# Optimization experiments

Measured on AMD Instinct MI355X. Metric: run time of the kernel, lower is better.

Reference implementation:

```python
import jax, jax.numpy as jnp
import numpy as np

NUM_HEADS = 16


def setup_inputs() -> dict:
    key = jax.random.key(0)
    ks = jax.random.split(key, 5)
    B, N, C = 4, 2048, 1024
    x = jax.random.normal(ks[0], (B, N, C), dtype=jnp.float32)
    mask = jax.random.randint(ks[1], (B, N), 0, 2, dtype=jnp.int32)
    W_qkv = jax.random.normal(ks[2], (C, 3 * C), dtype=jnp.float32) * (C ** -0.5)
    W_proj = jax.random.normal(ks[3], (C, C), dtype=jnp.float32) * (C ** -0.5)
    b_proj = jnp.zeros((C,), dtype=jnp.float32)
    return {"x": x, "mask": mask, "W_qkv": W_qkv, "W_proj": W_proj, "b_proj": b_proj}


def reference(x, mask, W_qkv, W_proj, b_proj):
    B, N, C = x.shape
    H = NUM_HEADS
    hd = C // H
    scale = hd ** -0.5
    # qkv projection -> [3, B, H, N, hd]
    qkv = (x @ W_qkv).reshape(B, N, 3, H, hd).transpose(2, 0, 3, 1, 4)
    q, k, v = qkv[0], qkv[1], qkv[2]
    attn = jnp.einsum('bhqd,bhkd->bhqk', q, k) * scale  # [B,H,N,N]
    add_mask = (mask[:, None, None, :] != 1).astype(jnp.float32) * -10000.0
    attn = jax.nn.softmax(attn + add_mask, axis=-1)
    out = jnp.einsum('bhqk,bhkd->bhqd', attn, v)  # [B,H,N,hd]
    out = out.transpose(0, 2, 1, 3).reshape(B, N, C)
    return out @ W_proj + b_proj
```

## Files before the change

### kernel.cpp

```cpp
#include <hip/hip_runtime.h>

typedef unsigned short u16;
typedef unsigned int u32;
typedef unsigned long long u64;
typedef __attribute__((ext_vector_type(8))) short short8;
typedef __attribute__((ext_vector_type(4))) float f32x4;

#define QSCALE 0.18033688f

__device__ __forceinline__ u16 f2bf(float f) {
  u32 u = __builtin_bit_cast(u32, f);
  u += 0x7fffu + ((u >> 16) & 1u);
  return (u16)(u >> 16);
}

__device__ __forceinline__ float fexp2(float x) {
#if __has_builtin(__builtin_amdgcn_exp2f)
  return __builtin_amdgcn_exp2f(x);
#else
  return exp2f(x);
#endif
}

__device__ __forceinline__ void glds16(u16* lds, const u16* g) {
  __builtin_amdgcn_global_load_lds(
      (const __attribute__((address_space(1))) u32*)g,
      (__attribute__((address_space(3))) u32*)lds, 16, 0, 0);
}

#define MFMA(a, b, c) __builtin_amdgcn_mfma_f32_16x16x32_bf16((a), (b), (c), 0, 0, 0)


__global__ __launch_bounds__(256) void prep(const float* __restrict__ x,
                                            const int* __restrict__ mask,
                                            const float* __restrict__ Wqkv,
                                            const float* __restrict__ Wproj,
                                            u16* __restrict__ xb,
                                            u16* __restrict__ wqkvt,
                                            u16* __restrict__ wprojt,
                                            int* __restrict__ s2t,
                                            int* __restrict__ nkbuf) {
  __shared__ float tile[64][65];
  __shared__ int wtot[4];
  __shared__ int wbase[5];
  const int bid = blockIdx.x, t = threadIdx.x;

  if (bid < 8192) {
    int i = bid * 256 + t;
    float4 v = ((const float4*)x)[i];
    union { u16 s[4]; u64 ll; } u;
    u.s[0] = f2bf(v.x); u.s[1] = f2bf(v.y); u.s[2] = f2bf(v.z); u.s[3] = f2bf(v.w);
    ((u64*)xb)[i] = u.ll;
    return;
  }
  if (bid < 9216) {
    const float* Wm; u16* Wt; int Cc, bj, bi;
    if (bid < 8960) { int tt = bid - 8192; Wm = Wqkv;  Wt = wqkvt;  Cc = 3072; bj = tt % 48; bi = tt / 48; }
    else            { int tt = bid - 8960; Wm = Wproj; Wt = wprojt; Cc = 1024; bj = tt & 15; bi = tt >> 4; }
    const int r = t >> 4, c4 = (t & 15) << 2;
    for (int rr = r; rr < 64; rr += 16) {
      float4 v = *(const float4*)&Wm[(size_t)(bi * 64 + rr) * Cc + bj * 64 + c4];
      tile[rr][c4] = v.x; tile[rr][c4 + 1] = v.y; tile[rr][c4 + 2] = v.z; tile[rr][c4 + 3] = v.w;
    }
    __syncthreads();
    for (int rr = r; rr < 64; rr += 16) {
      union { u16 s[4]; u64 ll; } u;
      u.s[0] = f2bf(tile[c4][rr]);
      u.s[1] = f2bf(tile[c4 + 1][rr]);
      u.s[2] = f2bf(tile[c4 + 2][rr]);
      u.s[3] = f2bf(tile[c4 + 3][rr]);
      *(u64*)&Wt[(size_t)(bj * 64 + rr) * 1024 + bi * 64 + c4] = u.ll;
    }
    return;
  }
  const int b = bid - 9216;
  const int lane = t & 63, w = t >> 6;
  int m8[8], c = 0;
  #pragma unroll
  for (int j = 0; j < 8; j++) {
    m8[j] = (mask[b * 2048 + t * 8 + j] == 1);
    c += m8[j];
  }
  int incl = c;
  #pragma unroll
  for (int off = 1; off < 64; off <<= 1) {
    int v = __shfl_up(incl, off);
    if (lane >= off) incl += v;
  }
  if (lane == 63) wtot[w] = incl;
  __syncthreads();
  if (t == 0) {
    int s = 0;
    for (int i = 0; i < 4; i++) { wbase[i] = s; s += wtot[i]; }
    wbase[4] = s;
  }
  __syncthreads();
  const int nk = wbase[4];
  int urun = wbase[w] + incl - c;
  #pragma unroll
  for (int j = 0; j < 8; j++) {
    int tok = t * 8 + j;
    int slot = m8[j] ? urun : nk + (tok - urun);
    s2t[b * 2048 + slot] = b * 2048 + tok;
    urun += m8[j];
  }
  if (t == 0) nkbuf[b] = nk;
}

__global__ __launch_bounds__(256, 4) void gemm_fused(const u16* __restrict__ xb,
                                                     const u16* __restrict__ wqkvt,
                                                     const int* __restrict__ s2t,
                                                     const int* __restrict__ nkbuf,
                                                     u16* __restrict__ qbuf,
                                                     u16* __restrict__ kc,
                                                     u16* __restrict__ vtc) {
  __shared__ u16 Asm[128 * 64];
  __shared__ u16 Bsm[128 * 64];
  const int bid = blockIdx.x;
  const int role = bid >> 9;
  const int sub = bid & 511;
  const int tid = threadIdx.x, lane = tid & 63, w = tid >> 6;
  const int quad = lane >> 4, l15 = lane & 15;
  const int wm = (w >> 1) * 64, wn = (w & 1) * 64;
  const int srow = lane >> 3;
  const int gcc = ((lane & 7) ^ srow) * 8;
  const int rx8 = (l15 & 7);

  int m0, n0;
  const u16 *Asrc, *Bsrc;
  if (role == 2) { m0 = (sub >> 6) * 128; n0 = (sub & 63) * 128; }
  else           { m0 = (sub & 63) * 128; n0 = (sub >> 6) * 128; }
  if (role == 1 && (m0 & 2047) >= nkbuf[m0 >> 11]) return;
  if (role == 2 && (n0 & 2047) >= nkbuf[n0 >> 11]) return;

  int arow[4], brow[4];
  #pragma unroll
  for (int c = 0; c < 4; ++c) {
    int rit = (w * 4 + c) * 8 + srow;
    if (role == 0)      { arow[c] = m0 + rit;            brow[c] = n0 + rit; }
    else if (role == 1) { arow[c] = s2t[m0 + rit];       brow[c] = 1024 + n0 + rit; }
    else                { arow[c] = 2048 + m0 + rit;     brow[c] = s2t[n0 + rit]; }
  }
  Asrc = (role == 2) ? wqkvt : xb;
  Bsrc = (role == 2) ? xb : wqkvt;

  f32x4 acc[4][4];
  #pragma unroll
  for (int i = 0; i < 4; i++)
    #pragma unroll
    for (int j = 0; j < 4; j++)
      #pragma unroll
      for (int r = 0; r < 4; r++) acc[i][j][r] = 0.f;

  for (int kt = 0; kt < 1024; kt += 64) {
    __syncthreads();
    #pragma unroll
    for (int c = 0; c < 4; ++c) {
      int chunk = w * 4 + c;
      glds16(&Asm[chunk * 512], &Asrc[(size_t)arow[c] * 1024 + kt + gcc]);
      glds16(&Bsm[chunk * 512], &Bsrc[(size_t)brow[c] * 1024 + kt + gcc]);
    }
    __syncthreads();
    #pragma unroll
    for (int ks = 0; ks < 2; ++ks) {
      int pc = ((ks * 4 + quad) ^ rx8) * 8;
      short8 av[4], bv[4];
      #pragma unroll
      for (int i = 0; i < 4; i++)
        av[i] = *(const short8*)&Asm[(wm + i * 16 + l15) * 64 + pc];
      #pragma unroll
      for (int j = 0; j < 4; j++)
        bv[j] = *(const short8*)&Bsm[(wn + j * 16 + l15) * 64 + pc];
      #pragma unroll
      for (int i = 0; i < 4; i++)
        #pragma unroll
        for (int j = 0; j < 4; j++)
          acc[i][j] = MFMA(av[i], bv[j], acc[i][j]);
    }
  }

  if (role == 2) {
    #pragma unroll
    for (int j = 0; j < 4; j++) {
      int col = n0 + wn + j * 16 + l15;
      int bb = col >> 11, sl = col & 2047;
      #pragma unroll
      for (int i = 0; i < 4; i++)
        #pragma unroll
        for (int r = 0; r < 4; r++) {
          int row = m0 + wm + i * 16 + quad * 4 + r;
          vtc[(size_t)(bb * 1024 + row) * 2048 + sl] = f2bf(acc[i][j][r]);
        }
    }
  } else {
    u16* dst = (role == 0) ? qbuf : kc;
    const float sc = (role == 0) ? QSCALE : 1.f;
    #pragma unroll
    for (int i = 0; i < 4; i++)
      #pragma unroll
      for (int j = 0; j < 4; j++) {
        int col = n0 + wn + j * 16 + l15;
        #pragma unroll
        for (int r = 0; r < 4; r++) {
          int row = m0 + wm + i * 16 + quad * 4 + r;
          dst[(size_t)row * 1024 + col] = f2bf(acc[i][j][r] * sc);
        }
      }
  }
}

__global__ __launch_bounds__(256, 2) void attn_kernel(const u16* __restrict__ q,
                                                      const u16* __restrict__ kc,
                                                      const u16* __restrict__ vtc,
                                                      const int* __restrict__ nkbuf,
                                                      u16* __restrict__ ao) {
  __shared__ u16 Ksm[2][64 * 64];
  __shared__ u16 Vsm[2][64 * 64];
  const int h = blockIdx.x, b = blockIdx.y, qt = blockIdx.z;
  const int tid = threadIdx.x, lane = tid & 63, w = tid >> 6;
  const int quad = lane >> 4, l15 = lane & 15;
  const int q0 = qt * 256 + w * 64;
  const int srow = lane >> 3;
  const int gcc = ((lane & 7) ^ srow) * 8;
  const int rx8 = (l15 & 7);
  const int nk = nkbuf[b];
  const int nt2 = (nk + 127) >> 7;
  const int quad8 = quad * 8;

  int vrow[2], prow[2];
  #pragma unroll
  for (int c = 0; c < 2; ++c) {
    int row = (w * 2 + c) * 8 + srow;
    vrow[c] = row;
    prow[c] = ((row >> 4) & 1) * 32 + ((row >> 2) & 3) * 8 + ((row >> 5) & 1) * 4 + (row & 3);
  }

  short8 ones;
  #pragma unroll
  for (int z = 0; z < 8; z++) ones[z] = (short)0x3F80;

  short8 qf[4][2];
  #pragma unroll
  for (int i = 0; i < 4; i++)
    #pragma unroll
    for (int ks = 0; ks < 2; ks++)
      qf[i][ks] = *(const short8*)&q[(size_t)(b * 2048 + q0 + i * 16 + l15) * 1024 +
                                     h * 64 + ks * 32 + quad * 8];

  f32x4 o[4][4], osum[4];
  #pragma unroll
  for (int i = 0; i < 4; i++) {
    #pragma unroll
    for (int r = 0; r < 4; r++) osum[i][r] = 0.f;
    #pragma unroll
    for (int jd = 0; jd < 4; jd++)
      #pragma unroll
      for (int r = 0; r < 4; r++) o[i][jd][r] = 0.f;
  }

#define SUBTILE(st_, kbase_)                                                           \
  {                                                                                    \
    f32x4 s[4][4];                                                                     \
    _Pragma("unroll") for (int j = 0; j < 4; j++)                                      \
      _Pragma("unroll") for (int i = 0; i < 4; i++)                                    \
        _Pragma("unroll") for (int r = 0; r < 4; r++) s[j][i][r] = 0.f;                \
    _Pragma("unroll") for (int ks = 0; ks < 2; ks++) {                                 \
      int pc = ((ks * 4 + quad) ^ rx8) * 8;                                            \
      short8 kf[4];                                                                    \
      _Pragma("unroll") for (int j = 0; j < 4; j++)                                    \
        kf[j] = *(const short8*)&Ksm[st_][(j * 16 + l15) * 64 + pc];                   \
      _Pragma("unroll") for (int j = 0; j < 4; j++)                                    \
        _Pragma("unroll") for (int i = 0; i < 4; i++)                                  \
          s[j][i] = MFMA(kf[j], qf[i][ks], s[j][i]);                                   \
    }                                                                                  \
    const bool tail = ((kbase_) + 64 > nk);                                            \
    short8 pf[4][2];                                                                   \
    _Pragma("unroll") for (int i = 0; i < 4; i++) {                                    \
      float p[4][4];                                                                   \
      if (!tail) {                                                                     \
        _Pragma("unroll") for (int j = 0; j < 4; j++)                                  \
          _Pragma("unroll") for (int r = 0; r < 4; r++)                                \
            p[j][r] = fexp2(s[j][i][r]);                                               \
      } else {                                                                         \
        _Pragma("unroll") for (int j = 0; j < 4; j++)                                  \
          _Pragma("unroll") for (int r = 0; r < 4; r++) {                              \
            int slot = (kbase_) + (j & 1) * 32 + quad8 + (j >> 1) * 4 + r;             \
            float e = fexp2(s[j][i][r]);                                               \
            p[j][r] = (slot < nk) ? e : 0.f;                                           \
          }                                                                            \
      }                                                                                \
      _Pragma("unroll") for (int ks = 0; ks < 2; ks++) {                               \
        union { u32 u[4]; short8 v; } pk;                                              \
        u32 a0 = __builtin_bit_cast(u32, p[ks][0]) + 0x8000u;                          \
        u32 a1 = __builtin_bit_cast(u32, p[ks][1]) + 0x8000u;                          \
        u32 a2 = __builtin_bit_cast(u32, p[ks][2]) + 0x8000u;                          \
        u32 a3 = __builtin_bit_cast(u32, p[ks][3]) + 0x8000u;                          \
        u32 b0 = __builtin_bit_cast(u32, p[ks + 2][0]) + 0x8000u;                      \
        u32 b1 = __builtin_bit_cast(u32, p[ks + 2][1]) + 0x8000u;                      \
        u32 b2 = __builtin_bit_cast(u32, p[ks + 2][2]) + 0x8000u;                      \
        u32 b3 = __builtin_bit_cast(u32, p[ks + 2][3]) + 0x8000u;                      \
        pk.u[0] = __builtin_amdgcn_perm(a1, a0, 0x07060302u);                          \
        pk.u[1] = __builtin_amdgcn_perm(a3, a2, 0x07060302u);                          \
        pk.u[2] = __builtin_amdgcn_perm(b1, b0, 0x07060302u);                          \
        pk.u[3] = __builtin_amdgcn_perm(b3, b2, 0x07060302u);                          \
        pf[i][ks] = pk.v;                                                              \
      }                                                                                \
    }                                                                                  \
    _Pragma("unroll") for (int ks = 0; ks < 2; ks++) {                                 \
      int pcv = ((ks * 4 + quad) ^ rx8) * 8;                                           \
      short8 vf[4];                                                                    \
      _Pragma("unroll") for (int jd = 0; jd < 4; jd++)                                 \
        vf[jd] = *(const short8*)&Vsm[st_][(jd * 16 + l15) * 64 + pcv];                \
      _Pragma("unroll") for (int i = 0; i < 4; i++) {                                  \
        osum[i] = MFMA(pf[i][ks], ones, osum[i]);                                      \
        _Pragma("unroll") for (int jd = 0; jd < 4; jd++)                               \
          o[i][jd] = MFMA(pf[i][ks], vf[jd], o[i][jd]);                                \
      }                                                                                \
    }                                                                                  \
  }

  for (int t = 0; t < nt2; ++t) {
    const int k0 = t * 128;
    __syncthreads();
    #pragma unroll
    for (int c = 0; c < 2; ++c) {
      int chunk = w * 2 + c;
      glds16(&Ksm[0][chunk * 512],
             &kc[(size_t)(b * 2048 + k0 + prow[c]) * 1024 + h * 64 + gcc]);
      glds16(&Vsm[0][chunk * 512],
             &vtc[(size_t)(b * 1024 + h * 64 + vrow[c]) * 2048 + k0 + gcc]);
      glds16(&Ksm[1][chunk * 512],
             &kc[(size_t)(b * 2048 + k0 + 64 + prow[c]) * 1024 + h * 64 + gcc]);
      glds16(&Vsm[1][chunk * 512],
             &vtc[(size_t)(b * 1024 + h * 64 + vrow[c]) * 2048 + k0 + 64 + gcc]);
    }
    __syncthreads();

    SUBTILE(0, k0)
    if (k0 + 64 < nk) SUBTILE(1, k0 + 64)
  }
#undef SUBTILE

  #pragma unroll
  for (int i = 0; i < 4; i++)
    #pragma unroll
    for (int r = 0; r < 4; r++) {
      float inv = 1.f / osum[i][r];
      size_t row = (size_t)(b * 2048 + q0 + i * 16 + quad * 4 + r);
      #pragma unroll
      for (int jd = 0; jd < 4; jd++)
        ao[row * 1024 + h * 64 + jd * 16 + l15] = f2bf(o[i][jd][r] * inv);
    }
}

__global__ __launch_bounds__(256, 3) void gemm_proj(const u16* __restrict__ A,
                                                    const u16* __restrict__ Bt,
                                                    const float* __restrict__ bias,
                                                    float* __restrict__ out) {
  __shared__ u16 Asm[128 * 64];
  __shared__ u16 Bsm[128 * 64];
  const int tid = threadIdx.x, lane = tid & 63, w = tid >> 6;
  const int quad = lane >> 4, l15 = lane & 15;
  const int m0 = (blockIdx.x & 63) * 128, n0 = (blockIdx.x >> 6) * 128;
  const int wm = (w >> 1) * 64, wn = (w & 1) * 64;
  const int srow = lane >> 3;
  const int gcc = ((lane & 7) ^ srow) * 8;
  const int rx8 = (l15 & 7);
  f32x4 acc[4][4];
  #pragma unroll
  for (int i = 0; i < 4; i++)
    #pragma unroll
    for (int j = 0; j < 4; j++)
      #pragma unroll
      for (int r = 0; r < 4; r++) acc[i][j][r] = 0.f;

  for (int kt = 0; kt < 1024; kt += 64) {
    __syncthreads();
    #pragma unroll
    for (int c = 0; c < 4; ++c) {
      int chunk = w * 4 + c;
      int row = chunk * 8 + srow;
      glds16(&Asm[chunk * 512], &A[(size_t)(m0 + row) * 1024 + kt + gcc]);
      glds16(&Bsm[chunk * 512], &Bt[(size_t)(n0 + row) * 1024 + kt + gcc]);
    }
    __syncthreads();
    #pragma unroll
    for (int ks = 0; ks < 2; ++ks) {
      int pc = ((ks * 4 + quad) ^ rx8) * 8;
      short8 av[4], bv[4];
      #pragma unroll
      for (int i = 0; i < 4; i++)
        av[i] = *(const short8*)&Asm[(wm + i * 16 + l15) * 64 + pc];
      #pragma unroll
      for (int j = 0; j < 4; j++)
        bv[j] = *(const short8*)&Bsm[(wn + j * 16 + l15) * 64 + pc];
      #pragma unroll
      for (int i = 0; i < 4; i++)
        #pragma unroll
        for (int j = 0; j < 4; j++)
          acc[i][j] = MFMA(av[i], bv[j], acc[i][j]);
    }
  }

  #pragma unroll
  for (int j = 0; j < 4; j++) {
    int col = n0 + wn + j * 16 + l15;
    float bj = bias[col];
    #pragma unroll
    for (int i = 0; i < 4; i++) {
      #pragma unroll
      for (int r = 0; r < 4; r++) {
        int row = m0 + wm + i * 16 + quad * 4 + r;
        out[(size_t)row * 1024 + col] = acc[i][j][r] + bj;
      }
    }
  }
}

extern "C" void kernel_launch(void* const* d_in, const int* in_sizes, int n_in,
                              void* d_out, int out_size, void* d_ws, size_t ws_size,
                              hipStream_t stream) {
  (void)in_sizes; (void)n_in; (void)out_size; (void)ws_size;
  const float* x     = (const float*)d_in[0];
  const int*   mask  = (const int*)d_in[1];
  const float* Wqkv  = (const float*)d_in[2];
  const float* Wproj = (const float*)d_in[3];
  const float* bproj = (const float*)d_in[4];
  float* out = (float*)d_out;
  char* ws = (char*)d_ws;

  size_t off = 0;
  u16* xb     = (u16*)(ws + off); off += 8192ull * 1024 * 2;
  u16* wqkvt  = (u16*)(ws + off); off += 3072ull * 1024 * 2;
  u16* wprojt = (u16*)(ws + off); off += 1024ull * 1024 * 2;
  u16* qbuf   = (u16*)(ws + off); off += 8192ull * 1024 * 2;
  u16* kcbuf  = (u16*)(ws + off); off += 4096ull * 2048 * 2;
  u16* vtcbuf = (u16*)(ws + off); off += 4096ull * 2048 * 2;
  int* s2t    = (int*)(ws + off); off += 8192ull * 4;
  int* nkbuf  = (int*)(ws + off); off += 4 * 4;
  u16* aobuf  = xb;

  prep<<<9220, 256, 0, stream>>>(x, mask, Wqkv, Wproj, xb, wqkvt, wprojt, s2t, nkbuf);
  gemm_fused<<<1536, 256, 0, stream>>>(xb, wqkvt, s2t, nkbuf, qbuf, kcbuf, vtcbuf);
  attn_kernel<<<dim3(16, 4, 8), 256, 0, stream>>>(qbuf, kcbuf, vtcbuf, nkbuf, aobuf);
  gemm_proj<<<512, 256, 0, stream>>>(aobuf, wprojt, bproj, out);
}
```

Measured before the change: 205.3 us.

## Rewrite QKV GEMM as 256x256 tile, 8-wave, double-buffered pipelined kernel

The fused QKV projection GEMM moves from 128x128 tiles with 4 waves and a single LDS buffer to 256x256 tiles with 8 waves (each wave covering 128x64). Global-to-LDS loads are double-buffered and staged one to two k-steps ahead, with explicit vmcnt waits, s_barrier and raised scheduling priority around the MFMA bursts. The goal is to overlap memory traffic with matrix math and to raise data reuse per tile. In exchange it uses 128KB of LDS and twice the accumulator registers, and launches far fewer blocks, which may hurt load balance and occupancy. Roles are now interleaved by bid % 3 instead of by block range.

Measured after the change: 221.9 us. 1.08x slower.

```diff
diff --git a/kernel.cpp b/kernel.cpp
--- a/kernel.cpp
+++ b/kernel.cpp
@@ -29,7 +29,6 @@
 }
 
 #define MFMA(a, b, c) __builtin_amdgcn_mfma_f32_16x16x32_bf16((a), (b), (c), 0, 0, 0)
-
 
 __global__ __launch_bounds__(256) void prep(const float* __restrict__ x,
                                             const int* __restrict__ mask,
@@ -107,77 +106,120 @@
   if (t == 0) nkbuf[b] = nk;
 }
 
-__global__ __launch_bounds__(256, 4) void gemm_fused(const u16* __restrict__ xb,
+
+#define GEMM8_DECLS \
+  const int tid = threadIdx.x, lane = tid & 63, w = tid >> 6; \
+  const int quad = lane >> 4, l15 = lane & 15; \
+  const int wm = (w >> 2) * 128, wn = (w & 3) * 64; \
+  const int psw8 = (quad ^ ((l15 >> 1) & 3)) * 8; \
+  const int li = w * 64 + lane; \
+  const int row0 = (li >> 2), row1 = 128 + (li >> 2); \
+  const int lc0 = (((li & 3) ^ ((row0 >> 1) & 3)) * 8);
+
+#define STAGE8(MAT, KH, T) { \
+  u16* reg_ = ldsb + (((((T) & 1) * 2 + (MAT)) * 2 + (KH)) * 8192); \
+  const u16* src_ = (MAT) ? Bsrc : Asrc; \
+  int r0_ = (MAT) ? brow0 : arow0, r1_ = (MAT) ? brow1 : arow1; \
+  int c_ = (T) * 64 + (KH) * 32 + lc0; \
+  glds16(reg_ + w * 512, &src_[(size_t)r0_ * 1024 + c_]); \
+  glds16(reg_ + 4096 + w * 512, &src_[(size_t)r1_ * 1024 + c_]); \
+}
+
+#define LOADA8(BUF, KS, IH) { \
+  const u16* reg_ = ldsb + ((((BUF) * 2 + 0) * 2 + (KS)) * 8192); \
+  _Pragma("unroll") for (int ii = 0; ii < 4; ++ii) \
+    av[ii] = *(const short8*)&reg_[(wm + ((IH) * 4 + ii) * 16 + l15) * 32 + psw8]; \
+}
+
+#define LOADB8(BUF, KS) { \
+  const u16* reg_ = ldsb + ((((BUF) * 2 + 1) * 2 + (KS)) * 8192); \
+  _Pragma("unroll") for (int j = 0; j < 4; ++j) \
+    bv[j] = *(const short8*)&reg_[(wn + j * 16 + l15) * 32 + psw8]; \
+}
+
+#define MFMA16X(IB) \
+  _Pragma("unroll") for (int ii = 0; ii < 4; ++ii) \
+    _Pragma("unroll") for (int j = 0; j < 4; ++j) \
+      acc[(IB) + ii][j] = MFMA(av[ii], bv[j], acc[(IB) + ii][j]);
+
+#define SBAR() asm volatile("s_barrier" ::: "memory")
+#define SGB0() __builtin_amdgcn_sched_barrier(0)
+
+#define GEMM8_CORE() { \
+  STAGE8(0, 0, 0) STAGE8(1, 0, 0) STAGE8(0, 1, 0) STAGE8(1, 1, 0) \
+  STAGE8(0, 0, 1) STAGE8(1, 0, 1) \
+  asm volatile("s_waitcnt vmcnt(4)" ::: "memory"); \
+  SBAR(); \
+  _Pragma("unroll 2") \
+  for (int t = 0; t < 16; ++t) { \
+    const int buf = t & 1; \
+    short8 av[4], bv[4]; \
+     \
+    LOADA8(buf, 0, 0) LOADB8(buf, 0) \
+    if (t + 1 < 16) STAGE8(0, 1, t + 1) \
+    SBAR(); SGB0(); \
+    __builtin_amdgcn_s_setprio(1); MFMA16X(0) __builtin_amdgcn_s_setprio(0); \
+    SBAR(); \
+     \
+    LOADA8(buf, 0, 1) \
+    if (t + 1 < 16) STAGE8(1, 1, t + 1) \
+    SBAR(); SGB0(); \
+    __builtin_amdgcn_s_setprio(1); MFMA16X(4) __builtin_amdgcn_s_setprio(0); \
+    SBAR(); \
+     \
+    LOADA8(buf, 1, 0) LOADB8(buf, 1) \
+    if (t + 2 < 16) STAGE8(0, 0, t + 2) \
+    SBAR(); SGB0(); \
+    __builtin_amdgcn_s_setprio(1); MFMA16X(0) __builtin_amdgcn_s_setprio(0); \
+    SBAR(); \
+     \
+    LOADA8(buf, 1, 1) \
+    if (t + 2 < 16) STAGE8(1, 0, t + 2) \
+    SBAR(); SGB0(); \
+    __builtin_amdgcn_s_setprio(1); MFMA16X(4) __builtin_amdgcn_s_setprio(0); \
+    if (t + 2 < 16) { asm volatile("s_waitcnt vmcnt(4)" ::: "memory"); } \
+    else            { asm volatile("s_waitcnt vmcnt(0)" ::: "memory"); } \
+    SBAR(); \
+  } \
+}
+
+__global__ __launch_bounds__(512, 2) void gemm_fused(const u16* __restrict__ xb,
                                                      const u16* __restrict__ wqkvt,
                                                      const int* __restrict__ s2t,
                                                      const int* __restrict__ nkbuf,
                                                      u16* __restrict__ qbuf,
                                                      u16* __restrict__ kc,
                                                      u16* __restrict__ vtc) {
-  __shared__ u16 Asm[128 * 64];
-  __shared__ u16 Bsm[128 * 64];
+  __shared__ u16 ldsb[65536];
   const int bid = blockIdx.x;
-  const int role = bid >> 9;
-  const int sub = bid & 511;
-  const int tid = threadIdx.x, lane = tid & 63, w = tid >> 6;
-  const int quad = lane >> 4, l15 = lane & 15;
-  const int wm = (w >> 1) * 64, wn = (w & 1) * 64;
-  const int srow = lane >> 3;
-  const int gcc = ((lane & 7) ^ srow) * 8;
-  const int rx8 = (l15 & 7);
-
+  const int role = bid % 3;
+  const int sub = bid / 3;
+  GEMM8_DECLS
   int m0, n0;
-  const u16 *Asrc, *Bsrc;
-  if (role == 2) { m0 = (sub >> 6) * 128; n0 = (sub & 63) * 128; }
-  else           { m0 = (sub & 63) * 128; n0 = (sub >> 6) * 128; }
+  if (role == 2) { m0 = (sub >> 5) * 256; n0 = (sub & 31) * 256; }
+  else           { m0 = (sub & 31) * 256; n0 = (sub >> 5) * 256; }
   if (role == 1 && (m0 & 2047) >= nkbuf[m0 >> 11]) return;
   if (role == 2 && (n0 & 2047) >= nkbuf[n0 >> 11]) return;
 
-  int arow[4], brow[4];
-  #pragma unroll
-  for (int c = 0; c < 4; ++c) {
-    int rit = (w * 4 + c) * 8 + srow;
-    if (role == 0)      { arow[c] = m0 + rit;            brow[c] = n0 + rit; }
-    else if (role == 1) { arow[c] = s2t[m0 + rit];       brow[c] = 1024 + n0 + rit; }
-    else                { arow[c] = 2048 + m0 + rit;     brow[c] = s2t[n0 + rit]; }
-  }
-  Asrc = (role == 2) ? wqkvt : xb;
-  Bsrc = (role == 2) ? xb : wqkvt;
-
-  f32x4 acc[4][4];
-  #pragma unroll
-  for (int i = 0; i < 4; i++)
+  int arow0, arow1, brow0, brow1;
+  if (role == 0)      { arow0 = m0 + row0;        arow1 = m0 + row1;
+                        brow0 = n0 + row0;        brow1 = n0 + row1; }
+  else if (role == 1) { arow0 = s2t[m0 + row0];   arow1 = s2t[m0 + row1];
+                        brow0 = 1024 + n0 + row0; brow1 = 1024 + n0 + row1; }
+  else                { arow0 = 2048 + m0 + row0; arow1 = 2048 + m0 + row1;
+                        brow0 = s2t[n0 + row0];   brow1 = s2t[n0 + row1]; }
+  const u16* Asrc = (role == 2) ? wqkvt : xb;
+  const u16* Bsrc = (role == 2) ? xb : wqkvt;
+
+  f32x4 acc[8][4];
+  #pragma unroll
+  for (int i = 0; i < 8; i++)
     #pragma unroll
     for (int j = 0; j < 4; j++)
       #pragma unroll
       for (int r = 0; r < 4; r++) acc[i][j][r] = 0.f;
 
-  for (int kt = 0; kt < 1024; kt += 64) {
-    __syncthreads();
-    #pragma unroll
-    for (int c = 0; c < 4; ++c) {
-      int chunk = w * 4 + c;
-      glds16(&Asm[chunk * 512], &Asrc[(size_t)arow[c] * 1024 + kt + gcc]);
-      glds16(&Bsm[chunk * 512], &Bsrc[(size_t)brow[c] * 1024 + kt + gcc]);
-    }
-    __syncthreads();
-    #pragma unroll
-    for (int ks = 0; ks < 2; ++ks) {
-      int pc = ((ks * 4 + quad) ^ rx8) * 8;
-      short8 av[4], bv[4];
-      #pragma unroll
-      for (int i = 0; i < 4; i++)
-        av[i] = *(const short8*)&Asm[(wm + i * 16 + l15) * 64 + pc];
-      #pragma unroll
-      for (int j = 0; j < 4; j++)
-        bv[j] = *(const short8*)&Bsm[(wn + j * 16 + l15) * 64 + pc];
-      #pragma unroll
-      for (int i = 0; i < 4; i++)
-        #pragma unroll
-        for (int j = 0; j < 4; j++)
-          acc[i][j] = MFMA(av[i], bv[j], acc[i][j]);
-    }
-  }
+  GEMM8_CORE()
 
   if (role == 2) {
     #pragma unroll
@@ -185,7 +227,7 @@
       int col = n0 + wn + j * 16 + l15;
       int bb = col >> 11, sl = col & 2047;
       #pragma unroll
-      for (int i = 0; i < 4; i++)
+      for (int i = 0; i < 8; i++)
         #pragma unroll
         for (int r = 0; r < 4; r++) {
           int row = m0 + wm + i * 16 + quad * 4 + r;
@@ -196,7 +238,7 @@
     u16* dst = (role == 0) ? qbuf : kc;
     const float sc = (role == 0) ? QSCALE : 1.f;
     #pragma unroll
-    for (int i = 0; i < 4; i++)
+    for (int i = 0; i < 8; i++)
       #pragma unroll
       for (int j = 0; j < 4; j++) {
         int col = n0 + wn + j * 16 + l15;
@@ -441,7 +483,7 @@
   u16* aobuf  = xb;
 
   prep<<<9220, 256, 0, stream>>>(x, mask, Wqkv, Wproj, xb, wqkvt, wprojt, s2t, nkbuf);
-  gemm_fused<<<1536, 256, 0, stream>>>(xb, wqkvt, s2t, nkbuf, qbuf, kcbuf, vtcbuf);
+  gemm_fused<<<384, 512, 0, stream>>>(xb, wqkvt, s2t, nkbuf, qbuf, kcbuf, vtcbuf);
   attn_kernel<<<dim3(16, 4, 8), 256, 0, stream>>>(qbuf, kcbuf, vtcbuf, nkbuf, aobuf);
   gemm_proj<<<512, 256, 0, stream>>>(aobuf, wprojt, bproj, out);
 }
```

## Double-buffer K/V and projection GEMM tiles in LDS, raise MFMA wave priority

Applied to the files above, without the earlier changes.

The attention kernel and the output-projection GEMM now hold two LDS buffers. The global-to-LDS load for the next tile is issued before computing on the current one, so the load at the top of each iteration is no longer serialized behind a barrier. In the attention kernel, s_setprio is raised around the MFMA blocks to favour waves that are issuing matrix work. The cost is doubled LDS per block: 64KB for both kernels. For gemm_proj this likely cuts occupancy below its launch bound of 3, which may offset some of the overlap.

New measurement: 206.4 us. Within noise of the previous version (+0.5%).

```diff
diff --git a/kernel.cpp b/kernel.cpp
--- a/kernel.cpp
+++ b/kernel.cpp
@@ -127,7 +127,6 @@
   const int rx8 = (l15 & 7);
 
   int m0, n0;
-  const u16 *Asrc, *Bsrc;
   if (role == 2) { m0 = (sub >> 6) * 128; n0 = (sub & 63) * 128; }
   else           { m0 = (sub & 63) * 128; n0 = (sub >> 6) * 128; }
   if (role == 1 && (m0 & 2047) >= nkbuf[m0 >> 11]) return;
@@ -141,8 +140,8 @@
     else if (role == 1) { arow[c] = s2t[m0 + rit];       brow[c] = 1024 + n0 + rit; }
     else                { arow[c] = 2048 + m0 + rit;     brow[c] = s2t[n0 + rit]; }
   }
-  Asrc = (role == 2) ? wqkvt : xb;
-  Bsrc = (role == 2) ? xb : wqkvt;
+  const u16 *Asrc = (role == 2) ? wqkvt : xb;
+  const u16 *Bsrc = (role == 2) ? xb : wqkvt;
 
   f32x4 acc[4][4];
   #pragma unroll
@@ -214,8 +213,8 @@
                                                       const u16* __restrict__ vtc,
                                                       const int* __restrict__ nkbuf,
                                                       u16* __restrict__ ao) {
-  __shared__ u16 Ksm[2][64 * 64];
-  __shared__ u16 Vsm[2][64 * 64];
+  __shared__ u16 Ksm[2][2][64 * 64];
+  __shared__ u16 Vsm[2][2][64 * 64];
   const int h = blockIdx.x, b = blockIdx.y, qt = blockIdx.z;
   const int tid = threadIdx.x, lane = tid & 63, w = tid >> 6;
   const int quad = lane >> 4, l15 = lane & 15;
@@ -258,7 +257,22 @@
       for (int r = 0; r < 4; r++) o[i][jd][r] = 0.f;
   }
 
-#define SUBTILE(st_, kbase_)                                                           \
+#define STAGEKV(pb_, t_) {                                                             \
+    const int k0s = (t_) * 128;                                                        \
+    _Pragma("unroll") for (int c = 0; c < 2; ++c) {                                    \
+      int chunk = w * 2 + c;                                                           \
+      glds16(&Ksm[pb_][0][chunk * 512],                                                \
+             &kc[(size_t)(b * 2048 + k0s + prow[c]) * 1024 + h * 64 + gcc]);           \
+      glds16(&Vsm[pb_][0][chunk * 512],                                                \
+             &vtc[(size_t)(b * 1024 + h * 64 + vrow[c]) * 2048 + k0s + gcc]);          \
+      glds16(&Ksm[pb_][1][chunk * 512],                                                \
+             &kc[(size_t)(b * 2048 + k0s + 64 + prow[c]) * 1024 + h * 64 + gcc]);      \
+      glds16(&Vsm[pb_][1][chunk * 512],                                                \
+             &vtc[(size_t)(b * 1024 + h * 64 + vrow[c]) * 2048 + k0s + 64 + gcc]);     \
+    }                                                                                  \
+  }
+
+#define SUBTILE(pb_, st_, kbase_)                                                      \
   {                                                                                    \
     f32x4 s[4][4];                                                                     \
     _Pragma("unroll") for (int j = 0; j < 4; j++)                                      \
@@ -268,10 +282,12 @@
       int pc = ((ks * 4 + quad) ^ rx8) * 8;                                            \
       short8 kf[4];                                                                    \
       _Pragma("unroll") for (int j = 0; j < 4; j++)                                    \
-        kf[j] = *(const short8*)&Ksm[st_][(j * 16 + l15) * 64 + pc];                   \
+        kf[j] = *(const short8*)&Ksm[pb_][st_][(j * 16 + l15) * 64 + pc];              \
+      __builtin_amdgcn_s_setprio(1);                                                   \
       _Pragma("unroll") for (int j = 0; j < 4; j++)                                    \
         _Pragma("unroll") for (int i = 0; i < 4; i++)                                  \
           s[j][i] = MFMA(kf[j], qf[i][ks], s[j][i]);                                   \
+      __builtin_amdgcn_s_setprio(0);                                                   \
     }                                                                                  \
     const bool tail = ((kbase_) + 64 > nk);                                            \
     short8 pf[4][2];                                                                   \
@@ -310,36 +326,29 @@
       int pcv = ((ks * 4 + quad) ^ rx8) * 8;                                           \
       short8 vf[4];                                                                    \
       _Pragma("unroll") for (int jd = 0; jd < 4; jd++)                                 \
-        vf[jd] = *(const short8*)&Vsm[st_][(jd * 16 + l15) * 64 + pcv];                \
+        vf[jd] = *(const short8*)&Vsm[pb_][st_][(jd * 16 + l15) * 64 + pcv];           \
+      __builtin_amdgcn_s_setprio(1);                                                   \
       _Pragma("unroll") for (int i = 0; i < 4; i++) {                                  \
         osum[i] = MFMA(pf[i][ks], ones, osum[i]);                                      \
         _Pragma("unroll") for (int jd = 0; jd < 4; jd++)                               \
           o[i][jd] = MFMA(pf[i][ks], vf[jd], o[i][jd]);                                \
       }                                                                                \
+      __builtin_amdgcn_s_setprio(0);                                                   \
     }                                                                                  \
   }
 
+  STAGEKV(0, 0)
+  __syncthreads();
   for (int t = 0; t < nt2; ++t) {
     const int k0 = t * 128;
+    const int pb = t & 1;
+    if (t + 1 < nt2) STAGEKV(pb ^ 1, t + 1)
+    SUBTILE(pb, 0, k0)
+    if (k0 + 64 < nk) SUBTILE(pb, 1, k0 + 64)
     __syncthreads();
-    #pragma unroll
-    for (int c = 0; c < 2; ++c) {
-      int chunk = w * 2 + c;
-      glds16(&Ksm[0][chunk * 512],
-             &kc[(size_t)(b * 2048 + k0 + prow[c]) * 1024 + h * 64 + gcc]);
-      glds16(&Vsm[0][chunk * 512],
-             &vtc[(size_t)(b * 1024 + h * 64 + vrow[c]) * 2048 + k0 + gcc]);
-      glds16(&Ksm[1][chunk * 512],
-             &kc[(size_t)(b * 2048 + k0 + 64 + prow[c]) * 1024 + h * 64 + gcc]);
-      glds16(&Vsm[1][chunk * 512],
-             &vtc[(size_t)(b * 1024 + h * 64 + vrow[c]) * 2048 + k0 + 64 + gcc]);
-    }
-    __syncthreads();
-
-    SUBTILE(0, k0)
-    if (k0 + 64 < nk) SUBTILE(1, k0 + 64)
   }
 #undef SUBTILE
+#undef STAGEKV
 
   #pragma unroll
   for (int i = 0; i < 4; i++)
@@ -357,8 +366,8 @@
                                                     const u16* __restrict__ Bt,
                                                     const float* __restrict__ bias,
                                                     float* __restrict__ out) {
-  __shared__ u16 Asm[128 * 64];
-  __shared__ u16 Bsm[128 * 64];
+  __shared__ u16 Asm[2][128 * 64];
+  __shared__ u16 Bsm[2][128 * 64];
   const int tid = threadIdx.x, lane = tid & 63, w = tid >> 6;
   const int quad = lane >> 4, l15 = lane & 15;
   const int m0 = (blockIdx.x & 63) * 128, n0 = (blockIdx.x >> 6) * 128;
@@ -374,33 +383,39 @@
       #pragma unroll
       for (int r = 0; r < 4; r++) acc[i][j][r] = 0.f;
 
-  for (int kt = 0; kt < 1024; kt += 64) {
-    __syncthreads();
-    #pragma unroll
-    for (int c = 0; c < 4; ++c) {
-      int chunk = w * 4 + c;
-      int row = chunk * 8 + srow;
-      glds16(&Asm[chunk * 512], &A[(size_t)(m0 + row) * 1024 + kt + gcc]);
-      glds16(&Bsm[chunk * 512], &Bt[(size_t)(n0 + row) * 1024 + kt + gcc]);
-    }
-    __syncthreads();
+#define STAGEP(pb_, kt_) {                                                             \
+    _Pragma("unroll") for (int c = 0; c < 4; ++c) {                                    \
+      int chunk = w * 4 + c;                                                           \
+      int row = chunk * 8 + srow;                                                      \
+      glds16(&Asm[pb_][chunk * 512], &A[(size_t)(m0 + row) * 1024 + (kt_) + gcc]);     \
+      glds16(&Bsm[pb_][chunk * 512], &Bt[(size_t)(n0 + row) * 1024 + (kt_) + gcc]);    \
+    }                                                                                  \
+  }
+
+  STAGEP(0, 0)
+  __syncthreads();
+  for (int kt = 0, t = 0; kt < 1024; kt += 64, ++t) {
+    const int pb = t & 1;
+    if (kt + 64 < 1024) STAGEP(pb ^ 1, kt + 64)
     #pragma unroll
     for (int ks = 0; ks < 2; ++ks) {
       int pc = ((ks * 4 + quad) ^ rx8) * 8;
       short8 av[4], bv[4];
       #pragma unroll
       for (int i = 0; i < 4; i++)
-        av[i] = *(const short8*)&Asm[(wm + i * 16 + l15) * 64 + pc];
+        av[i] = *(const short8*)&Asm[pb][(wm + i * 16 + l15) * 64 + pc];
       #pragma unroll
       for (int j = 0; j < 4; j++)
-        bv[j] = *(const short8*)&Bsm[(wn + j * 16 + l15) * 64 + pc];
+        bv[j] = *(const short8*)&Bsm[pb][(wn + j * 16 + l15) * 64 + pc];
       #pragma unroll
       for (int i = 0; i < 4; i++)
         #pragma unroll
         for (int j = 0; j < 4; j++)
           acc[i][j] = MFMA(av[i], bv[j], acc[i][j]);
     }
-  }
+    __syncthreads();
+  }
+#undef STAGEP
 
   #pragma unroll
   for (int j = 0; j < 4; j++) {
```
